# Performance work log

Hardware: AMD Instinct MI355X
Metric: run time of the kernel (lower is better)

## Reference

```python
import jax, jax.numpy as jnp
import numpy as np
from jax import lax

H_ENC = 64
H_DEC = 128
PRED_STEPS = 30


def _run_lstm_last(x, Wih, Whh, bih, bhh):
    """Batched LSTM (batch_first), returns last hidden state. x: [N, T, I] -> [N, H]."""
    N = x.shape[0]
    H = Whh.shape[1]
    xg = jnp.einsum('nti,gi->ntg', x, Wih) + bih  # [N, T, 4H], input projection hoisted

    def step(carry, g_t):
        h, c = carry
        gates = g_t + h @ Whh.T + bhh
        i, f, g, o = jnp.split(gates, 4, axis=-1)  # torch gate order i,f,g,o
        c = jax.nn.sigmoid(f) * c + jax.nn.sigmoid(i) * jnp.tanh(g)
        h = jax.nn.sigmoid(o) * jnp.tanh(c)
        return (h, c), None

    z = jnp.zeros((N, H), x.dtype)
    (h, _), _ = lax.scan(step, (z, z), jnp.swapaxes(xg, 0, 1))
    return h


def setup_inputs() -> dict:
    key = jax.random.key(0)
    ks = jax.random.split(key, 20)
    B, T, NMAX = 2048, 50, 16
    s = 0.1
    inp = {
        'train_agent': jax.random.normal(ks[0], (B, T, 2), jnp.float32),
        'neighbour': jax.random.normal(ks[1], (B, NMAX, T, 2), jnp.float32),
        'neighbour_counts': jax.random.randint(ks[2], (B,), 0, NMAX + 1),
        # agent encoder LSTM(2 -> 64)
        'Wih_a': jax.random.normal(ks[3], (4 * H_ENC, 2), jnp.float32) * s,
        'Whh_a': jax.random.normal(ks[4], (4 * H_ENC, H_ENC), jnp.float32) * s,
        'bih_a': jax.random.normal(ks[5], (4 * H_ENC,), jnp.float32) * s,
        'bhh_a': jax.random.normal(ks[6], (4 * H_ENC,), jnp.float32) * s,
        # neighbour encoder LSTM(2 -> 64)
        'Wih_n': jax.random.normal(ks[7], (4 * H_ENC, 2), jnp.float32) * s,
        'Whh_n': jax.random.normal(ks[8], (4 * H_ENC, H_ENC), jnp.float32) * s,
        'bih_n': jax.random.normal(ks[9], (4 * H_ENC,), jnp.float32) * s,
        'bhh_n': jax.random.normal(ks[10], (4 * H_ENC,), jnp.float32) * s,
        # decoder LSTMCell(128 -> 128)
        'Wih_d': jax.random.normal(ks[11], (4 * H_DEC, H_DEC), jnp.float32) * s,
        'Whh_d': jax.random.normal(ks[12], (4 * H_DEC, H_DEC), jnp.float32) * s,
        'bih_d': jax.random.normal(ks[13], (4 * H_DEC,), jnp.float32) * s,
        'bhh_d': jax.random.normal(ks[14], (4 * H_DEC,), jnp.float32) * s,
        # embedding_pos Linear(128 -> 2)
        'Wpos': jax.random.normal(ks[15], (2, H_DEC), jnp.float32) * s,
        'bpos': jax.random.normal(ks[16], (2,), jnp.float32) * s,
    }
    return inp


def reference(train_agent, neighbour, neighbour_counts,
              Wih_a, Whh_a, bih_a, bhh_a,
              Wih_n, Whh_n, bih_n, bhh_n,
              Wih_d, Whh_d, bih_d, bhh_d,
              Wpos, bpos):
    B, NMAX, T, _ = neighbour.shape

    # agent encoder: last hidden state  [B, 64]
    agent_emb = _run_lstm_last(train_agent, Wih_a, Whh_a, bih_a, bhh_a)

    # neighbour encoder over all padded neighbour sequences  [B*NMAX, 64]
    n_enc = _run_lstm_last(neighbour.reshape(B * NMAX, T, 2),
                           Wih_n, Whh_n, bih_n, bhh_n).reshape(B, NMAX, H_ENC)
    valid = jnp.arange(NMAX)[None, :] < neighbour_counts[:, None]  # [B, NMAX]
    neg_inf = jnp.asarray(-jnp.inf, n_enc.dtype)
    n_max = jnp.max(jnp.where(valid[:, :, None], n_enc, neg_inf), axis=1)  # [B, 64]
    neigh_emb = jnp.where((neighbour_counts > 0)[:, None], n_max,
                          jnp.zeros((), n_enc.dtype))

    # decoder: LSTMCell fed its own hidden state as input, 30 steps
    h0 = jnp.concatenate([agent_emb, neigh_emb], axis=1)  # [B, 128]
    c0 = jnp.zeros_like(h0)

    def dec_step(carry, _):
        h, c = carry
        gates = h @ Wih_d.T + bih_d + h @ Whh_d.T + bhh_d  # input == hidden == h
        i, f, g, o = jnp.split(gates, 4, axis=-1)
        c_new = jax.nn.sigmoid(f) * c + jax.nn.sigmoid(i) * jnp.tanh(g)
        h_new = jax.nn.sigmoid(o) * jnp.tanh(c_new)
        pred = h_new @ Wpos.T + bpos  # [B, 2]
        return (h_new, c_new), pred

    _, preds = lax.scan(dec_step, (h0, c0), None, length=PRED_STEPS)  # [30, B, 2]
    return jnp.swapaxes(preds, 0, 1)  # [B, 30, 2]
```

## Files before the change

kernel.cpp:

```cpp
#include <hip/hip_runtime.h>
#include <stdint.h>


#define T_SEQ 50
#define PRED_STEPS 30
#define NMAX 16

typedef float v2f __attribute__((ext_vector_type(2)));
typedef float v4f __attribute__((ext_vector_type(4)));
typedef short v8s __attribute__((ext_vector_type(8)));

#define L2E 1.44269504f
#define L2E2 2.88539008f

static constexpr size_t OFF_AEMB  = 0;
static constexpr size_t OFF_NENC  = 131072;
static constexpr size_t OFF_PACKA = 2490368;
static constexpr size_t OFF_PACKN = 2498560;
static constexpr size_t OFF_WDP   = 2506752;
static constexpr size_t OFF_WDB   = 2539520;

__device__ __forceinline__ float frcp(float x) { return __builtin_amdgcn_rcpf(x); }
#if __has_builtin(__builtin_amdgcn_exp2f)
__device__ __forceinline__ float fexp2(float x) { return __builtin_amdgcn_exp2f(x); }
#else
__device__ __forceinline__ float fexp2(float x) { return exp2f(x); }
#endif
__device__ __forceinline__ unsigned bf16rne(float f) {
  unsigned u = __float_as_uint(f);
  u += 0x7fff + ((u >> 16) & 1);
  return u >> 16;
}
__device__ __forceinline__ v4f mfma16(v8s a, v8s b, v4f c) {
  return __builtin_amdgcn_mfma_f32_16x16x32_bf16(a, b, c, 0, 0, 0);
}

__device__ __forceinline__ float cell_update(float iv, float fv, float gv,
                                             float ov, float& cref) {
  float ef = fexp2(-fv);
  float ei = fexp2(-iv);
  float eg = fexp2(-gv);
  float t1 = (1.f + ei) * (1.f + eg);
  float rD = frcp((1.f + ef) * t1);
  float sf = t1 * rD;
  float u  = (1.f - eg) * ((1.f + ef) * rD);
  float cn = fmaf(sf, cref, u);
  cref = cn;
  float eo = fexp2(-ov);
  float ec = fexp2(fminf(-L2E2 * cn, 60.f));
  return (1.f - ec) * frcp((1.f + eo) * (1.f + ec));
}

__device__ __forceinline__ uint4 pack8(const float* __restrict__ p, float gs) {
  float4 w0 = *(const float4*)p;
  float4 w1 = *(const float4*)(p + 4);
  uint4 o;
  o.x = bf16rne(w0.x * gs) | (bf16rne(w0.y * gs) << 16);
  o.y = bf16rne(w0.z * gs) | (bf16rne(w0.w * gs) << 16);
  o.z = bf16rne(w1.x * gs) | (bf16rne(w1.y * gs) << 16);
  o.w = bf16rne(w1.z * gs) | (bf16rne(w1.w * gs) << 16);
  return o;
}
__device__ __forceinline__ uint4 pack8sum(const float* __restrict__ pa,
                                          const float* __restrict__ pb, float gs) {
  float4 a0 = *(const float4*)pa, a1 = *(const float4*)(pa + 4);
  float4 b0 = *(const float4*)pb, b1 = *(const float4*)(pb + 4);
  uint4 o;
  o.x = bf16rne((a0.x + b0.x) * gs) | (bf16rne((a0.y + b0.y) * gs) << 16);
  o.y = bf16rne((a0.z + b0.z) * gs) | (bf16rne((a0.w + b0.w) * gs) << 16);
  o.z = bf16rne((a1.x + b1.x) * gs) | (bf16rne((a1.y + b1.y) * gs) << 16);
  o.w = bf16rne((a1.z + b1.z) * gs) | (bf16rne((a1.w + b1.w) * gs) << 16);
  return o;
}

__global__ void prep_kernel(const float* __restrict__ Whh_a, const float* __restrict__ Whh_n,
                            const float* __restrict__ Wih_d, const float* __restrict__ Whh_d,
                            const float* __restrict__ bih_d, const float* __restrict__ bhh_d,
                            uint4* __restrict__ packA, uint4* __restrict__ packN,
                            uint4* __restrict__ packD, float* __restrict__ bd) {
  const int b = blockIdx.x;
  if (b < 16) {
    const int which = b >> 3;
    const float* Whh = which ? Whh_n : Whh_a;
    uint4* dst = which ? packN : packA;
    const int idx = (b & 7) * 256 + threadIdx.x;
    const int lane = idx & 63, c = idx >> 6;
    const int kh = c & 1, g = (c >> 1) & 3, w = c >> 3;
    const float gs = (g == 2) ? L2E2 : L2E;
    const int row = g * 64 + 16 * w + (lane & 15);
    const int kb = kh * 32 + (lane >> 4) * 8;
    dst[c * 64 + lane] = pack8(Whh + row * 64 + kb, gs);
  } else {
    const int idx = (b - 16) * 256 + threadIdx.x;
    const int lane = idx & 63, c = idx >> 6;
    const int kh = c & 3, i = (c >> 2) & 1, wv = c >> 3;
    const int g = wv & 3, q = wv >> 2;
    const float gs = (g == 2) ? L2E2 : L2E;
    const int ju = q * 32 + i * 16 + (lane & 15);
    const int row = g * 128 + ju;
    const int kb = kh * 32 + (lane >> 4) * 8;
    packD[c * 64 + lane] = pack8sum(Wih_d + row * 128 + kb, Whh_d + row * 128 + kb, gs);
    if (b < 18) {
      int iB = (b - 16) * 256 + threadIdx.x;
      float s = ((iB >> 7) == 2) ? L2E2 : L2E;
      bd[iB] = (bih_d[iB] + bhh_d[iB]) * s;
    }
  }
}

__global__ __launch_bounds__(256, 4) void enc_mfma_kernel(
    const float* __restrict__ xA, const float* __restrict__ xN,
    const v8s* __restrict__ packA, const v8s* __restrict__ packN,
    const float* __restrict__ Wih_a, const float* __restrict__ bih_a, const float* __restrict__ bhh_a,
    const float* __restrict__ Wih_n, const float* __restrict__ bih_n, const float* __restrict__ bhh_n,
    float* __restrict__ outA, float* __restrict__ outN) {
  __shared__ unsigned short hph[2304];
  __shared__ float xst[1600];
  const int tid = threadIdx.x, lane = tid & 63, wv = tid >> 6;
  const int nb = blockIdx.x;
  const bool isA = nb >= 2048;
  const float* xsrc = isA ? xA : xN;
  const v8s* pk = isA ? packA : packN;
  const float* Wih = isA ? Wih_a : Wih_n;
  const float* bih = isA ? bih_a : bih_n;
  const float* bhh = isA ? bhh_a : bhh_n;
  float* outp = isA ? outA : outN;
  const int s0 = (isA ? nb - 2048 : nb) * 16;

  v8s B[4][2];
#pragma unroll
  for (int g = 0; g < 4; ++g)
#pragma unroll
    for (int kh = 0; kh < 2; ++kh)
      B[g][kh] = pk[(wv * 8 + g * 2 + kh) * 64 + lane];

  const int jc = lane & 15, qc = lane >> 4;
  float wi0[4], wi1[4], bs[4];
#pragma unroll
  for (int g = 0; g < 4; ++g) {
    const float gs = (g == 2) ? L2E2 : L2E;
    int n = g * 64 + 16 * wv + jc;
    wi0[g] = Wih[n * 2 + 0] * gs;
    wi1[g] = Wih[n * 2 + 1] * gs;
    bs[g] = (bih[n] + bhh[n]) * gs;
  }

  {
    const float4* xb = (const float4*)(xsrc + (size_t)s0 * 100);
    for (int i = tid; i < 400; i += 256) ((float4*)xst)[i] = xb[i];
    for (int i = tid; i < 576; i += 256) ((unsigned*)hph)[i] = 0;
  }
  __syncthreads();

  const int ms = lane & 15, ks = lane >> 4;
  float cst[4] = {0.f, 0.f, 0.f, 0.f};
  float h[4];

  auto enc_step = [&](int t, int rb, int wb) {
    v4f a4[4];
#pragma unroll
    for (int r = 0; r < 4; ++r) {
      v2f xv = *(const __shared__ v2f*)&xst[(qc * 4 + r) * 100 + 2 * t];
#pragma unroll
      for (int g = 0; g < 4; ++g)
        a4[g][r] = fmaf(wi1[g], xv.y, fmaf(wi0[g], xv.x, bs[g]));
    }

#pragma unroll
    for (int kh = 0; kh < 2; ++kh) {
      v8s Ahi = *(const __shared__ v8s*)&hph[rb + ms * 72 + kh * 32 + ks * 8];
#pragma unroll
      for (int g = 0; g < 4; ++g)
        a4[g] = mfma16(Ahi, B[g][kh], a4[g]);
    }

#pragma unroll
    for (int r = 0; r < 4; ++r) {
      h[r] = cell_update(a4[0][r], a4[1][r], a4[2][r], a4[3][r], cst[r]);
      hph[wb + (qc * 4 + r) * 72 + 16 * wv + jc] =
          (unsigned short)bf16rne(h[r]);
    }
    __syncthreads();
  };

  for (int t2 = 0; t2 < T_SEQ; t2 += 2) {
    enc_step(t2 + 0, 0, 1152);
    enc_step(t2 + 1, 1152, 0);
  }

#pragma unroll
  for (int r = 0; r < 4; ++r)
    outp[(size_t)(s0 + qc * 4 + r) * 64 + 16 * wv + jc] = h[r];
}

__global__ __launch_bounds__(1024, 4) void dec_mfma_kernel(
    const v8s* __restrict__ pkd, const float* __restrict__ bd,
    const float* __restrict__ aemb, const float* __restrict__ nenc,
    const int* __restrict__ cnts, const float* __restrict__ Wpos,
    const float* __restrict__ bpos, float* __restrict__ out) {
  __shared__ unsigned short hph[2176];
  __shared__ float gbuf[4][8][132];
  __shared__ float ppart[16][2];
  __shared__ float pbuf[480];
  const int tid = threadIdx.x, lane = tid & 63, wv = tid >> 6;
  const int jc = lane & 15, qc = lane >> 4;
  const int g = wv & 3, q = wv >> 2;
  const int s0 = blockIdx.x * 8;

  v8s B[2][4];
  float bs[2];
#pragma unroll
  for (int i = 0; i < 2; ++i) {
#pragma unroll
    for (int kh = 0; kh < 4; ++kh)
      B[i][kh] = pkd[(wv * 8 + i * 4 + kh) * 64 + lane];
    bs[i] = bd[g * 128 + q * 32 + i * 16 + jc];
  }

  const int cu = (wv & 1) * 64 + lane;
  const int sq = wv >> 1;
  const float wp0 = Wpos[cu], wp1 = Wpos[128 + cu];
  const float bp0 = bpos[0], bp1 = bpos[1];

  for (int i = tid; i < 2048; i += 1024) {
    int row = i >> 7, unit = i & 127;
    unsigned hiw = 0;
    if (row < 8) {
      float v;
      if (unit < 64) {
        v = aemb[(size_t)(s0 + row) * 64 + unit];
      } else {
        int cnt = cnts[s0 + row];
        float m = -1e30f;
#pragma unroll
        for (int n = 0; n < NMAX; ++n) {
          float val = nenc[((size_t)((s0 + row) * NMAX + n)) * 64 + (unit - 64)];
          m = (n < cnt) ? fmaxf(m, val) : m;
        }
        v = (cnt > 0) ? m : 0.f;
      }
      hiw = bf16rne(v);
    }
    hph[row * 136 + unit] = (unsigned short)hiw;
  }
  float cst = 0.f;
  __syncthreads();

  for (int t = 0; t < PRED_STEPS; ++t) {
    v4f acc[2];
#pragma unroll
    for (int i = 0; i < 2; ++i)
      acc[i] = (v4f){bs[i], bs[i], bs[i], bs[i]};
#pragma unroll
    for (int kh = 0; kh < 4; ++kh) {
      v8s Ahi = *(const __shared__ v8s*)&hph[jc * 136 + kh * 32 + qc * 8];
#pragma unroll
      for (int i = 0; i < 2; ++i)
        acc[i] = mfma16(Ahi, B[i][kh], acc[i]);
    }

    if (qc < 2) {
#pragma unroll
      for (int i = 0; i < 2; ++i)
#pragma unroll
        for (int r = 0; r < 4; ++r)
          gbuf[g][qc * 4 + r][q * 32 + i * 16 + jc] = acc[i][r];
    }
    __syncthreads();

    float gI = gbuf[0][sq][cu];
    float gF = gbuf[1][sq][cu];
    float gG = gbuf[2][sq][cu];
    float gO = gbuf[3][sq][cu];
    float h = cell_update(gI, gF, gG, gO, cst);

    hph[sq * 136 + cu] = (unsigned short)bf16rne(h);

    float p0 = h * wp0;
    float p1 = h * wp1;
#pragma unroll
    for (int off = 32; off > 0; off >>= 1) {
      p0 += __shfl_xor(p0, off, 64);
      p1 += __shfl_xor(p1, off, 64);
    }
    if (lane == 0) { ppart[wv][0] = p0; ppart[wv][1] = p1; }
    __syncthreads();

    if (tid < 16) {
      int s = tid >> 1, cc = tid & 1;
      pbuf[s * 60 + t * 2 + cc] =
          ppart[2 * s][cc] + ppart[2 * s + 1][cc] + (cc ? bp1 : bp0);
    }
  }
  __syncthreads();
  if (tid < 480) out[(size_t)s0 * 60 + tid] = pbuf[tid];
}

extern "C" void kernel_launch(void* const* d_in, const int* in_sizes, int n_in,
                              void* d_out, int out_size, void* d_ws, size_t ws_size,
                              hipStream_t stream) {
  (void)in_sizes; (void)n_in; (void)out_size; (void)ws_size;
  const float* xA    = (const float*)d_in[0];
  const float* xN    = (const float*)d_in[1];
  const int*   cnts  = (const int*)d_in[2];
  const float* Wih_a = (const float*)d_in[3];
  const float* Whh_a = (const float*)d_in[4];
  const float* bih_a = (const float*)d_in[5];
  const float* bhh_a = (const float*)d_in[6];
  const float* Wih_n = (const float*)d_in[7];
  const float* Whh_n = (const float*)d_in[8];
  const float* bih_n = (const float*)d_in[9];
  const float* bhh_n = (const float*)d_in[10];
  const float* Wih_d = (const float*)d_in[11];
  const float* Whh_d = (const float*)d_in[12];
  const float* bih_d = (const float*)d_in[13];
  const float* bhh_d = (const float*)d_in[14];
  const float* Wpos  = (const float*)d_in[15];
  const float* bpos  = (const float*)d_in[16];
  float* out = (float*)d_out;
  float* wsf = (float*)d_ws;

  prep_kernel<<<48, 256, 0, stream>>>(Whh_a, Whh_n, Wih_d, Whh_d, bih_d, bhh_d,
                                      (uint4*)(wsf + OFF_PACKA),
                                      (uint4*)(wsf + OFF_PACKN),
                                      (uint4*)(wsf + OFF_WDP), wsf + OFF_WDB);
  enc_mfma_kernel<<<2176, 256, 0, stream>>>(
      xA, xN,
      (const v8s*)(wsf + OFF_PACKA), (const v8s*)(wsf + OFF_PACKN),
      Wih_a, bih_a, bhh_a, Wih_n, bih_n, bhh_n,
      wsf + OFF_AEMB, wsf + OFF_NENC);
  dec_mfma_kernel<<<256, 1024, 0, stream>>>(
      (const v8s*)(wsf + OFF_WDP), wsf + OFF_WDB,
      wsf + OFF_AEMB, wsf + OFF_NENC, cnts,
      Wpos, bpos, out);
}
```

Measured before the change: 269.0 us.

## Compact valid neighbours and skip encoder work for padded neighbour slots

Adds a compaction kernel that atomically builds a list of valid (batch, neighbour) indices from neighbour_counts. Neighbour encoder blocks beyond the compacted count exit early, and the remaining blocks gather their inputs and scatter outputs by index. This removes LSTM work for masked neighbours, at the cost of an extra launch, an atomic, and gathered loads. The output order becomes nondeterministic, but each index is written to its own slot.

```diff
diff --git a/kernel.cpp b/kernel.cpp
--- a/kernel.cpp
+++ b/kernel.cpp
@@ -15,6 +15,7 @@
 
 static constexpr size_t OFF_AEMB  = 0;
 static constexpr size_t OFF_NENC  = 131072;
+static constexpr size_t OFF_IDX   = 2228224;
 static constexpr size_t OFF_PACKA = 2490368;
 static constexpr size_t OFF_PACKN = 2498560;
 static constexpr size_t OFF_WDP   = 2506752;
@@ -77,8 +78,14 @@
                             const float* __restrict__ Wih_d, const float* __restrict__ Whh_d,
                             const float* __restrict__ bih_d, const float* __restrict__ bhh_d,
                             uint4* __restrict__ packA, uint4* __restrict__ packN,
-                            uint4* __restrict__ packD, float* __restrict__ bd) {
+                            uint4* __restrict__ packD, float* __restrict__ bd,
+                            int* __restrict__ idxb) {
   const int b = blockIdx.x;
+  {
+    const int gi = b * 256 + threadIdx.x;
+    for (int i = gi; i < 32768; i += 12288) idxb[i] = -1;
+    if (gi == 0) idxb[32768] = 0;
+  }
   if (b < 16) {
     const int which = b >> 3;
     const float* Whh = which ? Whh_n : Whh_a;
@@ -108,24 +115,39 @@
   }
 }
 
+__global__ void compact_kernel(const int* __restrict__ cnts, int* __restrict__ idxb) {
+  const int b = blockIdx.x * 256 + threadIdx.x;
+  if (b >= 2048) return;
+  int cnt = cnts[b];
+  cnt = cnt < 0 ? 0 : (cnt > NMAX ? NMAX : cnt);
+  if (cnt == 0) return;
+  int pos = atomicAdd(idxb + 32768, cnt);
+  for (int j = 0; j < cnt; ++j) idxb[pos + j] = b * NMAX + j;
+}
+
 __global__ __launch_bounds__(256, 4) void enc_mfma_kernel(
     const float* __restrict__ xA, const float* __restrict__ xN,
     const v8s* __restrict__ packA, const v8s* __restrict__ packN,
     const float* __restrict__ Wih_a, const float* __restrict__ bih_a, const float* __restrict__ bhh_a,
     const float* __restrict__ Wih_n, const float* __restrict__ bih_n, const float* __restrict__ bhh_n,
+    const int* __restrict__ idxb,
     float* __restrict__ outA, float* __restrict__ outN) {
   __shared__ unsigned short hph[2304];
   __shared__ float xst[1600];
+  __shared__ int sidx[16];
   const int tid = threadIdx.x, lane = tid & 63, wv = tid >> 6;
   const int nb = blockIdx.x;
   const bool isA = nb >= 2048;
+  const int s0 = (isA ? nb - 2048 : nb) * 16;
+
+  if (!isA && s0 >= idxb[32768]) return;
+
   const float* xsrc = isA ? xA : xN;
   const v8s* pk = isA ? packA : packN;
   const float* Wih = isA ? Wih_a : Wih_n;
   const float* bih = isA ? bih_a : bih_n;
   const float* bhh = isA ? bhh_a : bhh_n;
   float* outp = isA ? outA : outN;
-  const int s0 = (isA ? nb - 2048 : nb) * 16;
 
   v8s B[4][2];
 #pragma unroll
@@ -146,9 +168,15 @@
   }
 
   {
-    const float4* xb = (const float4*)(xsrc + (size_t)s0 * 100);
-    for (int i = tid; i < 400; i += 256) ((float4*)xst)[i] = xb[i];
+    if (tid < 16) sidx[tid] = isA ? (s0 + tid) : idxb[s0 + tid];
     for (int i = tid; i < 576; i += 256) ((unsigned*)hph)[i] = 0;
+    __syncthreads();
+    for (int i = tid; i < 400; i += 256) {
+      int slot = i / 25, j = i - slot * 25;
+      int sq = sidx[slot];
+      const float4* xb = (const float4*)(xsrc + (size_t)(sq < 0 ? 0 : sq) * 100);
+      ((float4*)xst)[i] = xb[j];
+    }
   }
   __syncthreads();
 
@@ -189,8 +217,11 @@
   }
 
 #pragma unroll
-  for (int r = 0; r < 4; ++r)
-    outp[(size_t)(s0 + qc * 4 + r) * 64 + 16 * wv + jc] = h[r];
+  for (int r = 0; r < 4; ++r) {
+    int sq = sidx[qc * 4 + r];
+    if (sq >= 0)
+      outp[(size_t)sq * 64 + 16 * wv + jc] = h[r];
+  }
 }
 
 __global__ __launch_bounds__(1024, 4) void dec_mfma_kernel(
@@ -319,15 +350,18 @@
   const float* bpos  = (const float*)d_in[16];
   float* out = (float*)d_out;
   float* wsf = (float*)d_ws;
+  int* idxb = (int*)(wsf + OFF_IDX);
 
   prep_kernel<<<48, 256, 0, stream>>>(Whh_a, Whh_n, Wih_d, Whh_d, bih_d, bhh_d,
                                       (uint4*)(wsf + OFF_PACKA),
                                       (uint4*)(wsf + OFF_PACKN),
-                                      (uint4*)(wsf + OFF_WDP), wsf + OFF_WDB);
+                                      (uint4*)(wsf + OFF_WDP), wsf + OFF_WDB,
+                                      idxb);
+  compact_kernel<<<8, 256, 0, stream>>>(cnts, idxb);
   enc_mfma_kernel<<<2176, 256, 0, stream>>>(
       xA, xN,
       (const v8s*)(wsf + OFF_PACKA), (const v8s*)(wsf + OFF_PACKN),
-      Wih_a, bih_a, bhh_a, Wih_n, bih_n, bhh_n,
+      Wih_a, bih_a, bhh_a, Wih_n, bih_n, bhh_n, idxb,
       wsf + OFF_AEMB, wsf + OFF_NENC);
   dec_mfma_kernel<<<256, 1024, 0, stream>>>(
       (const v8s*)(wsf + OFF_WDP), wsf + OFF_WDB,
```

After: 220.2 us. 1.22x faster.
